# Kernel tuning notes

Measured on AMD Instinct MI355X. Metric: run time of the kernel, lower is better.

## Reference

```python
import jax, jax.numpy as jnp
import numpy as np

N = 262144          # flattened tokens (batch * seq)
D = 256             # bert_hidden_units
C = 50001           # num_items + 1


def setup_inputs() -> dict:
    key = jax.random.key(0)
    k1, k2, k3, k4 = jax.random.split(key, 4)
    inputs_row = jax.random.normal(k1, (N, D), dtype=jnp.float32)
    center = jax.random.normal(k2, (C, D), dtype=jnp.float32)
    target_row = jax.random.randint(k3, (N,), 0, C, dtype=jnp.int64)
    target = jax.random.randint(k4, (4096,), 0, C, dtype=jnp.int64)
    return {"inputs_row": inputs_row, "center": center,
            "target_row": target_row, "target": target}


def reference(inputs_row, center, target_row, target):
    # Fused scatter-mean replacement of the per-class Python loop:
    # for i in unique(target): center[i] = mean(inputs_row[target_row == i])
    num_classes = center.shape[0]
    sums = jax.ops.segment_sum(inputs_row, target_row, num_segments=num_classes)          # [C, D]
    counts = jax.ops.segment_sum(jnp.ones((inputs_row.shape[0],), inputs_row.dtype),
                                 target_row, num_segments=num_classes)                   # [C]
    mean = sums / jnp.where(counts > 0, counts, 1.0)[:, None]                            # [C, D]
    # only classes appearing in `target` are considered, and only those with
    # a nonzero row_mask (counts > 0) actually overwrite center[i]
    present = jnp.zeros((num_classes,), dtype=bool).at[target].set(True)
    upd = present & (counts > 0)
    return jnp.where(upd[:, None], mean, center)
```

## Files before the change

kernel.cpp:

```cpp
#include <hip/hip_runtime.h>

#define N_TOK 262144
#define DDIM  256
#define CCLS  50001

__global__ void build_kernel(const int* __restrict__ trow,
                             int* __restrict__ heads,
                             int* __restrict__ next) {
    int i = blockIdx.x * blockDim.x + threadIdx.x;
    if (i < N_TOK) {
        const int t = trow[i];
        const int old = atomicExch(&heads[t], i);
        next[i] = old;
    }
}

__global__ void update_kernel(const float* __restrict__ in,
                              const int* __restrict__ tgt, int n_tgt,
                              const int* __restrict__ heads,
                              const int* __restrict__ next,
                              float* __restrict__ out) {
    const int wid  = threadIdx.x >> 6;
    const int lane = threadIdx.x & 63;
    const int i = blockIdx.x * 4 + wid;
    if (i >= n_tgt) return;

    const int c = tgt[i];
    const int head = heads[c];
    if (head == -1) return;

    float4 acc = {0.f, 0.f, 0.f, 0.f};
    int cnt = 0;
    for (int row = head; row != -1; row = next[row]) {
        const float4 v =
            reinterpret_cast<const float4*>(in)[(long long)row * (DDIM / 4) + lane];
        acc.x += v.x; acc.y += v.y; acc.z += v.z; acc.w += v.w;
        ++cnt;
    }
    const float inv = 1.0f / (float)cnt;
    float4 r;
    r.x = acc.x * inv; r.y = acc.y * inv; r.z = acc.z * inv; r.w = acc.w * inv;
    reinterpret_cast<float4*>(out)[(long long)c * (DDIM / 4) + lane] = r;
}

extern "C" void kernel_launch(void* const* d_in, const int* in_sizes, int n_in,
                              void* d_out, int out_size, void* d_ws, size_t ws_size,
                              hipStream_t stream) {
    const float* inputs_row = (const float*)d_in[0];
    const float* center     = (const float*)d_in[1];
    const int*   target_row = (const int*)d_in[2];
    const int*   target     = (const int*)d_in[3];
    const int    n_target   = in_sizes[3];

    float* out = (float*)d_out;

    int* heads = (int*)d_ws;
    int* next  = heads + CCLS;

    hipMemsetAsync(heads, 0xFF, (size_t)CCLS * sizeof(int), stream);

    build_kernel<<<(N_TOK + 255) / 256, 256, 0, stream>>>(target_row, heads, next);

    hipMemcpyAsync(out, center, (size_t)CCLS * DDIM * sizeof(float),
                   hipMemcpyDeviceToDevice, stream);

    update_kernel<<<(n_target + 3) / 4, 256, 0, stream>>>(inputs_row, target, n_target,
                                                          heads, next, out);
}
```

Before: 48.54 us.

## Fuse linked-list build with center copy into one kernel

Merges the per-token head/next linked-list build and the 51 MB center-to-output copy into a single 2048-block kernel. Each block handles 128 tokens and a contiguous slab of the copy using nontemporal loads and stores, which removes a separate memcpy launch. The list now uses 1-based indices so heads can be zeroed with a plain memset, and the next-pointer load is issued before the accumulate to overlap the pointer chase. The risk is that half of each block's threads sit idle during the build step, and the copy is now bound to the block count.

Result: slower. 50.28 us (+3.6%).

```diff
diff --git a/kernel.cpp b/kernel.cpp
--- a/kernel.cpp
+++ b/kernel.cpp
@@ -3,15 +3,38 @@
 #define N_TOK 262144
 #define DDIM  256
 #define CCLS  50001
+#define ROW4  (DDIM / 4)
+#define NBLK  2048
+#define NTHR  256
+#define ROWS_PER_BLK (N_TOK / NBLK)
+#define TOTAL4 ((long long)CCLS * ROW4)
+#define SLAB   ((TOTAL4 + NBLK - 1) / NBLK)
 
-__global__ void build_kernel(const int* __restrict__ trow,
-                             int* __restrict__ heads,
-                             int* __restrict__ next) {
-    int i = blockIdx.x * blockDim.x + threadIdx.x;
-    if (i < N_TOK) {
+typedef __attribute__((ext_vector_type(4))) float f4;
+
+__global__ __launch_bounds__(NTHR)
+void build_copy_kernel(const int* __restrict__ trow,
+                       int* __restrict__ heads,
+                       int* __restrict__ next,
+                       const float* __restrict__ center,
+                       float* __restrict__ out) {
+    const int tid = threadIdx.x;
+
+    if (tid < ROWS_PER_BLK) {
+        const int i = blockIdx.x * ROWS_PER_BLK + tid;
         const int t = trow[i];
-        const int old = atomicExch(&heads[t], i);
+        const int old = atomicExch(&heads[t], i + 1);
         next[i] = old;
+    }
+
+    const long long base = (long long)blockIdx.x * SLAB;
+    long long end = base + SLAB;
+    if (end > TOTAL4) end = TOTAL4;
+    const f4* __restrict__ src = reinterpret_cast<const f4*>(center);
+    f4* __restrict__ dst = reinterpret_cast<f4*>(out);
+    for (long long j = base + tid; j < end; j += NTHR) {
+        f4 v = __builtin_nontemporal_load(&src[j]);
+        __builtin_nontemporal_store(v, &dst[j]);
     }
 }
 
@@ -26,21 +49,22 @@
     if (i >= n_tgt) return;
 
     const int c = tgt[i];
-    const int head = heads[c];
-    if (head == -1) return;
+    int r = heads[c];
+    if (r == 0) return;
 
     float4 acc = {0.f, 0.f, 0.f, 0.f};
     int cnt = 0;
-    for (int row = head; row != -1; row = next[row]) {
+    while (r != 0) {
+        const int row = r - 1;
         const float4 v =
-            reinterpret_cast<const float4*>(in)[(long long)row * (DDIM / 4) + lane];
+            reinterpret_cast<const float4*>(in)[(long long)row * ROW4 + lane];
+        r = next[row];
         acc.x += v.x; acc.y += v.y; acc.z += v.z; acc.w += v.w;
         ++cnt;
     }
-    const float inv = 1.0f / (float)cnt;
-    float4 r;
-    r.x = acc.x * inv; r.y = acc.y * inv; r.z = acc.z * inv; r.w = acc.w * inv;
-    reinterpret_cast<float4*>(out)[(long long)c * (DDIM / 4) + lane] = r;
+    const float s = 1.0f / (float)cnt;
+    float4 m = {acc.x * s, acc.y * s, acc.z * s, acc.w * s};
+    reinterpret_cast<float4*>(out)[(long long)c * ROW4 + lane] = m;
 }
 
 extern "C" void kernel_launch(void* const* d_in, const int* in_sizes, int n_in,
@@ -57,12 +81,9 @@
     int* heads = (int*)d_ws;
     int* next  = heads + CCLS;
 
-    hipMemsetAsync(heads, 0xFF, (size_t)CCLS * sizeof(int), stream);
+    hipMemsetAsync(heads, 0, (size_t)CCLS * sizeof(int), stream);
 
-    build_kernel<<<(N_TOK + 255) / 256, 256, 0, stream>>>(target_row, heads, next);
-
-    hipMemcpyAsync(out, center, (size_t)CCLS * DDIM * sizeof(float),
-                   hipMemcpyDeviceToDevice, stream);
+    build_copy_kernel<<<NBLK, NTHR, 0, stream>>>(target_row, heads, next, center, out);
 
     update_kernel<<<(n_target + 3) / 4, 256, 0, stream>>>(inputs_row, target, n_target,
                                                           heads, next, out);
```
